# Kernel tuning notes

Hardware: AMD Instinct MI355X
Metric: run time of the kernel (lower is better)

The kernel has to match this reference:

```python
import jax, jax.numpy as jnp
import numpy as np

N_NODES = 100000
N_EDGES = 1600000
D_IN = 128
D_HID = 128
N_GRAPHS = 128


def setup_inputs() -> dict:
    key = jax.random.key(0)
    ks = jax.random.split(key, 6)
    x = jax.random.normal(ks[0], (N_NODES, D_IN), dtype=jnp.float32)
    edge_index = jax.random.randint(ks[1], (2, N_EDGES), 0, N_NODES, dtype=jnp.int32)
    batch = jnp.sort(jax.random.randint(ks[2], (N_NODES,), 0, N_GRAPHS, dtype=jnp.int32))
    # GCNConv params (glorot-ish weight, zero bias), PReLU slope init 0.25 per channel
    W = jax.random.normal(ks[3], (D_IN, D_HID), dtype=jnp.float32) / np.float32(np.sqrt(D_IN))
    b = jnp.zeros((D_HID,), dtype=jnp.float32)
    prelu_a = jnp.full((D_HID,), 0.25, dtype=jnp.float32)
    return {"x": x, "edge_index": edge_index, "batch": batch, "W": W, "b": b, "prelu_a": prelu_a}


def reference(x, edge_index, batch, W, b, prelu_a):
    n_nodes = x.shape[0]
    # ---- GCNConv: add self-loops, symmetric deg^-1/2 normalization ----
    h = x @ W  # [N, H]
    loop = jnp.arange(n_nodes, dtype=edge_index.dtype)
    src = jnp.concatenate([edge_index[0], loop])  # [E+N]
    dst = jnp.concatenate([edge_index[1], loop])
    deg = jax.ops.segment_sum(jnp.ones_like(dst, jnp.float32), dst, num_segments=n_nodes)
    dinv = jnp.where(deg > 0, jax.lax.rsqrt(deg), 0.0)  # deg^-1/2 (inf -> 0, as in PyG)
    norm = dinv[src] * dinv[dst]  # [E+N]
    msg = h[src] * norm[:, None]  # gather + scale
    out = jax.ops.segment_sum(msg, dst, num_segments=n_nodes) + b  # scatter-add
    # ---- PReLU (per-channel slope) ----
    out = jnp.where(out > 0, out, prelu_a * out)
    # ---- F.normalize: L2 over dim=1, eps=1e-12 ----
    nrm = jnp.sqrt(jnp.sum(out * out, axis=1, keepdims=True))
    out = out / jnp.maximum(nrm, 1e-12)
    # ---- global_mean_pool over batch ids ----
    cnt = jax.ops.segment_sum(jnp.ones((n_nodes,), jnp.float32), batch, num_segments=N_GRAPHS)
    pooled = jax.ops.segment_sum(out, batch, num_segments=N_GRAPHS) / jnp.maximum(cnt, 1.0)[:, None]
    return pooled  # [N_GRAPHS, D_HID]
```

## Files before the change

kernel.cpp:

```cpp
#include <hip/hip_runtime.h>

#define D 128
#define NG 128
#define CAP 64
#define BIN 128
#define EPB 8192
#define NBMAX 1024

typedef unsigned short ushort_t;
typedef __bf16 bf16x8 __attribute__((ext_vector_type(8)));
typedef float floatx4 __attribute__((ext_vector_type(4)));

static __device__ __forceinline__ unsigned short f2bf(float f) {
    unsigned u = __float_as_uint(f);
    unsigned r = (u + 0x7fffu + ((u >> 16) & 1u)) >> 16;
    return (unsigned short)r;
}
static __device__ __forceinline__ float bflo(unsigned v) { return __uint_as_float(v << 16); }
static __device__ __forceinline__ float bfhi(unsigned v) { return __uint_as_float(v & 0xffff0000u); }
static __device__ __forceinline__ void acc2(float2& a, unsigned v) {
    a.x += __uint_as_float(v << 16);
    a.y += __uint_as_float(v & 0xffff0000u);
}

__global__ __launch_bounds__(256) void k_init(const float* __restrict__ W, ushort_t* __restrict__ Wp,
                                              const int* __restrict__ batch, int N,
                                              float* __restrict__ cntinv, float* __restrict__ out,
                                              int* __restrict__ cursor, int nb, int cap) {
    int t = blockIdx.x * 256 + threadIdx.x;
    int T = gridDim.x * 256;
    for (int i = t; i < NG * D; i += T) out[i] = 0.f;
    for (int b = t; b < nb; b += T) cursor[b] = b * cap;
    if (blockIdx.x == 0) {
        int tid = threadIdx.x;
        for (int i = tid; i < D * D; i += 256) {
            int c = i >> 7, k = i & 127;
            Wp[i] = f2bf(W[k * D + c]);
        }
        if (tid < NG) {
            int g = tid;
            int lo = 0, hi = N;
            while (lo < hi) { int mid = (lo + hi) >> 1; if (batch[mid] < g) lo = mid + 1; else hi = mid; }
            int a = lo;
            hi = N;
            while (lo < hi) { int mid = (lo + hi) >> 1; if (batch[mid] < g + 1) lo = mid + 1; else hi = mid; }
            int c = lo - a;
            cntinv[g] = 1.0f / (float)(c > 1 ? c : 1);
        }
    }
}

__global__ __launch_bounds__(256) void k_ascatter(const int* __restrict__ src, const int* __restrict__ dst,
                                                  int E, int nb, int* __restrict__ cursor,
                                                  int* __restrict__ ebuf) {
    __shared__ int hist[NBMAX];
    __shared__ int curs[NBMAX];
    int tid = threadIdx.x;
    for (int i = tid; i < nb; i += 256) hist[i] = 0;
    __syncthreads();
    int base = blockIdx.x * EPB;
    int cnt = E - base; if (cnt > EPB) cnt = EPB;
    for (int k = tid; k < cnt; k += 256) {
        atomicAdd(&hist[(unsigned)dst[base + k] >> 7], 1);
    }
    __syncthreads();
    for (int i = tid; i < nb; i += 256) {
        int v = hist[i];
        curs[i] = v ? atomicAdd(&cursor[i], v) : 0;
    }
    __syncthreads();
    for (int k = tid; k < cnt; k += 256) {
        int dv = dst[base + k];
        int sv = src[base + k];
        int pos = atomicAdd(&curs[dv >> 7], 1);
        ebuf[pos] = (sv << 7) | ((dv & 127) << 24);
    }
}

__global__ __launch_bounds__(256) void k_bucket(int* __restrict__ ebuf, const int* __restrict__ cursor,
                                                int cap, int N, int* __restrict__ rs, int* __restrict__ deg) {
    __shared__ int lists[BIN * CAP];
    __shared__ int lcnt[BIN];
    __shared__ int lpos[BIN];
    int tid = threadIdx.x;
    int b = blockIdx.x;
    for (int i = tid; i < BIN; i += 256) lcnt[i] = 0;
    __syncthreads();
    int s = b * cap;
    int e = cursor[b];
    for (int i = s + tid; i < e; i += 256) {
        int pk = ebuf[i];
        int n = (unsigned)pk >> 24;
        int pos = atomicAdd(&lcnt[n], 1);
        if (pos < CAP) lists[n * CAP + pos] = pk & 0xFFFFFF;
    }
    __syncthreads();
    int c0 = (tid < BIN) ? min(lcnt[tid], CAP) : 0;
    if (tid < BIN) lpos[tid] = c0;
    __syncthreads();
    for (int off = 1; off < BIN; off <<= 1) {
        int tv = 0;
        if (tid < BIN && tid >= off) tv = lpos[tid - off];
        __syncthreads();
        if (tid < BIN) lpos[tid] += tv;
        __syncthreads();
    }
    int n0 = b * BIN;
    if (tid < BIN) {
        int node = n0 + tid;
        if (node < N) { rs[node] = s + lpos[tid] - c0; deg[node] = c0; }
    }
    __syncthreads();
    {
        int n = tid >> 1, hf = tid & 1;
        int c = min(lcnt[n], CAP);
        int wbase = s + lpos[n] - c;
        for (int k = hf; k < c; k += 2) ebuf[wbase + k] = lists[n * CAP + k] << 1;
    }
}

__global__ __launch_bounds__(256) void k_gemm(const float* __restrict__ x, const ushort_t* __restrict__ Wp,
                                              const int* __restrict__ deg, ushort_t* __restrict__ h, int N) {
    __shared__ ushort_t smem[64 * 132 + 128 * 128];
    ushort_t* xs = smem;
    ushort_t* ws = smem + 64 * 132;

    const int tid = threadIdx.x;
    const int w = tid >> 6;
    const int lane = tid & 63;
    const int q = lane >> 4;
    const int m = lane & 15;
    const int row0 = blockIdx.x * 64;

#pragma unroll
    for (int it = 0; it < 8; ++it) {
        int i = it * 256 + tid;
        int r = i >> 5, s = i & 31;
        int row = row0 + r;
        uint2 pk;
        if (row < N) {
            float4 v = *(const float4*)&x[(size_t)row * D + s * 4];
            pk.x = (unsigned)f2bf(v.x) | ((unsigned)f2bf(v.y) << 16);
            pk.y = (unsigned)f2bf(v.z) | ((unsigned)f2bf(v.w) << 16);
        } else {
            pk.x = 0; pk.y = 0;
        }
        int off = (s * 8) ^ ((r & 7) << 4);
        *(uint2*)((char*)xs + r * 256 + off) = pk;
    }
#pragma unroll
    for (int it = 0; it < 8; ++it) {
        int i = it * 256 + tid;
        int c = i >> 4, s = i & 15;
        bf16x8 v = *(const bf16x8*)(Wp + (size_t)c * D + s * 8);
        int off = (s * 16) ^ ((c & 7) << 4);
        *(bf16x8*)((char*)ws + c * 256 + off) = v;
    }
    __syncthreads();

    floatx4 acc[8];
#pragma unroll
    for (int nt = 0; nt < 8; ++nt) acc[nt] = (floatx4){0.f, 0.f, 0.f, 0.f};

    const int arow_l = w * 16 + m;
    const int swz = (m & 7) << 4;
#pragma unroll
    for (int kb = 0; kb < 4; ++kb) {
        const int koff = (kb * 64 + q * 16) ^ swz;
        const bf16x8 av = *(const bf16x8*)((const char*)xs + arow_l * 256 + koff);
#pragma unroll
        for (int nt = 0; nt < 8; ++nt) {
            int c = nt * 16 + m;
            const bf16x8 bv = *(const bf16x8*)((const char*)ws + c * 256 + koff);
            acc[nt] = __builtin_amdgcn_mfma_f32_16x16x32_bf16(av, bv, acc[nt], 0, 0, 0);
        }
    }

    float di[4];
#pragma unroll
    for (int r = 0; r < 4; ++r) {
        int row = row0 + w * 16 + q * 4 + r;
        di[r] = (row < N) ? rsqrtf((float)(deg[row] + 1)) : 0.f;
    }
    __syncthreads();

#pragma unroll
    for (int nt = 0; nt < 8; ++nt) {
#pragma unroll
        for (int r = 0; r < 4; ++r) {
            xs[(w * 16 + q * 4 + r) * 132 + nt * 16 + m] = f2bf(acc[nt][r] * di[r]);
        }
    }
    __syncthreads();
#pragma unroll
    for (int it = 0; it < 8; ++it) {
        int i = it * 256 + tid;
        int r = i >> 5, s = i & 31;
        int row = row0 + r;
        if (row < N) {
            *(uint2*)&h[(size_t)row * D + s * 4] = *(const uint2*)&xs[r * 132 + s * 4];
        }
    }
}

__global__ __launch_bounds__(256) void k_gather(const ushort_t* __restrict__ h,
                                                const int* __restrict__ rs, const int* __restrict__ deg,
                                                const int* __restrict__ ebuf,
                                                const int* __restrict__ batch, const float* __restrict__ b,
                                                const float* __restrict__ pa, const float* __restrict__ cntinv,
                                                float* __restrict__ out, int N) {
    __shared__ float rows[4][128];
    __shared__ int gids[4];
    const int wave = threadIdx.x >> 6;
    const int lane = threadIdx.x & 63;
    const int half = lane >> 5;
    const int fl = lane & 31;
    const int node = blockIdx.x * 4 + wave;
    const int nodeC = (node < N) ? node : (N - 1);
    const bool valid = (node < N);
    const char* hb = (const char*)h;
    const unsigned flb = (unsigned)fl * 8;

    float2 a01 = {0.f, 0.f}, a23 = {0.f, 0.f};

    int start = valid ? rs[nodeC] : 0;
    int len = valid ? deg[nodeC] : 0;
    {
        int m = len;
        int idx = (lane < len) ? ebuf[start + lane] : 0;
        int j = 0;
        for (; j + 8 <= m; j += 8) {
            unsigned o0 = (unsigned)__shfl(idx, j + half) + flb;
            unsigned o1 = (unsigned)__shfl(idx, j + 2 + half) + flb;
            unsigned o2 = (unsigned)__shfl(idx, j + 4 + half) + flb;
            unsigned o3 = (unsigned)__shfl(idx, j + 6 + half) + flb;
            uint2 v0 = *(const uint2*)(hb + o0);
            uint2 v1 = *(const uint2*)(hb + o1);
            uint2 v2 = *(const uint2*)(hb + o2);
            uint2 v3 = *(const uint2*)(hb + o3);
            acc2(a01, v0.x); acc2(a23, v0.y);
            acc2(a01, v1.x); acc2(a23, v1.y);
            acc2(a01, v2.x); acc2(a23, v2.y);
            acc2(a01, v3.x); acc2(a23, v3.y);
        }
        for (; j + 2 <= m; j += 2) {
            unsigned o0 = (unsigned)__shfl(idx, j + half) + flb;
            uint2 v0 = *(const uint2*)(hb + o0);
            acc2(a01, v0.x); acc2(a23, v0.y);
        }
        if (j < m) {
            unsigned o0 = (unsigned)__shfl(idx, j) + flb;
            if (half == 0) {
                uint2 v0 = *(const uint2*)(hb + o0);
                acc2(a01, v0.x); acc2(a23, v0.y);
            }
        }
    }

    a01.x += __shfl_xor(a01.x, 32);
    a01.y += __shfl_xor(a01.y, 32);
    a23.x += __shfl_xor(a23.x, 32);
    a23.y += __shfl_xor(a23.y, 32);

    uint2 sv = *(const uint2*)&h[(size_t)nodeC * D + fl * 4];
    acc2(a01, sv.x); acc2(a23, sv.y);

    float dinv = rsqrtf((float)(len + 1));
    float4 bb = *(const float4*)&b[fl * 4];
    float4 aa = *(const float4*)&pa[fl * 4];
    float v0 = a01.x * dinv + bb.x;
    float v1 = a01.y * dinv + bb.y;
    float v2 = a23.x * dinv + bb.z;
    float v3 = a23.y * dinv + bb.w;
    v0 = v0 > 0.f ? v0 : aa.x * v0;
    v1 = v1 > 0.f ? v1 : aa.y * v1;
    v2 = v2 > 0.f ? v2 : aa.z * v2;
    v3 = v3 > 0.f ? v3 : aa.w * v3;
    float ss = v0 * v0 + v1 * v1 + v2 * v2 + v3 * v3;
#pragma unroll
    for (int o = 16; o > 0; o >>= 1) ss += __shfl_xor(ss, o);
    float inv = valid ? (1.0f / fmaxf(sqrtf(ss), 1e-12f)) : 0.f;

    if (half == 0) {
        *(float4*)&rows[wave][fl * 4] = make_float4(v0 * inv, v1 * inv, v2 * inv, v3 * inv);
        if (fl == 0) gids[wave] = batch[nodeC];
    }
    __syncthreads();

    if (threadIdx.x < 128) {
        int f = threadIdx.x;
        float acc = rows[0][f];
        int g = gids[0];
#pragma unroll
        for (int i = 1; i < 4; ++i) {
            int gi = gids[i];
            float vv = rows[i][f];
            if (gi == g) {
                acc += vv;
            } else {
                atomicAdd(&out[(size_t)g * D + f], acc * cntinv[g]);
                g = gi;
                acc = vv;
            }
        }
        atomicAdd(&out[(size_t)g * D + f], acc * cntinv[g]);
    }
}

extern "C" void kernel_launch(void* const* d_in, const int* in_sizes, int n_in,
                              void* d_out, int out_size, void* d_ws, size_t ws_size,
                              hipStream_t stream) {
    const float* x = (const float*)d_in[0];
    const int* ei = (const int*)d_in[1];
    const int* batch = (const int*)d_in[2];
    const float* W = (const float*)d_in[3];
    const float* b = (const float*)d_in[4];
    const float* pa = (const float*)d_in[5];
    float* out = (float*)d_out;

    const int N = in_sizes[0] / D;
    const int E = in_sizes[1] / 2;
    const int* src = ei;
    const int* dst = ei + E;

    const int nb = (N + BIN - 1) / BIN;
    const int nblk = (E + EPB - 1) / EPB;
    const int mean = (E + nb - 1) / nb;
    const int cap = mean + mean / 5 + 512;

    char* w = (char*)d_ws;
    auto carve = [&](size_t bytes) {
        void* p = (void*)w;
        w += (bytes + 255) & ~(size_t)255;
        return p;
    };
    ushort_t* h = (ushort_t*)carve((size_t)N * D * sizeof(ushort_t));
    ushort_t* Wp = (ushort_t*)carve((size_t)D * D * sizeof(ushort_t));
    int* deg = (int*)carve((size_t)N * sizeof(int));
    int* rs = (int*)carve((size_t)N * sizeof(int));
    int* ebuf = (int*)carve((size_t)nb * cap * sizeof(int));
    int* cursor = (int*)carve(NBMAX * sizeof(int));
    float* cntinv = (float*)carve(NG * sizeof(float));

    k_init<<<32, 256, 0, stream>>>(W, Wp, batch, N, cntinv, out, cursor, nb, cap);
    k_ascatter<<<nblk, 256, 0, stream>>>(src, dst, E, nb, cursor, ebuf);
    k_bucket<<<nb, 256, 0, stream>>>(ebuf, cursor, cap, N, rs, deg);
    k_gemm<<<(N + 63) / 64, 256, 0, stream>>>(x, Wp, deg, h, N);
    k_gather<<<(N + 3) / 4, 256, 0, stream>>>(h, rs, deg, ebuf, batch, b, pa, cntinv, out, N);
}
```

Before: 244.4 us.

## Pad edge lists to multiples of eight and map one node per half-wave

The bucket kernel now pads each node's edge list to a multiple of 8 entries. The padding entries point to an extra all-zero row appended to h, which k_init clears. The gather kernel assigns one node to each 32-lane half-wave, so a block handles 8 nodes. Every node then runs fixed 8-wide unrolled load batches with no tail handling and no cross-half reduction. The change also halves edges per scatter block, runs the bucket kernel with 512 threads, and enlarges the per-bin capacity to make room for the padding, at the cost of extra loads of the dummy row.

```diff
diff --git a/kernel.cpp b/kernel.cpp
--- a/kernel.cpp
+++ b/kernel.cpp
@@ -4,7 +4,7 @@
 #define NG 128
 #define CAP 64
 #define BIN 128
-#define EPB 8192
+#define EPB 4096
 #define NBMAX 1024
 
 typedef unsigned short ushort_t;
@@ -16,8 +16,6 @@
     unsigned r = (u + 0x7fffu + ((u >> 16) & 1u)) >> 16;
     return (unsigned short)r;
 }
-static __device__ __forceinline__ float bflo(unsigned v) { return __uint_as_float(v << 16); }
-static __device__ __forceinline__ float bfhi(unsigned v) { return __uint_as_float(v & 0xffff0000u); }
 static __device__ __forceinline__ void acc2(float2& a, unsigned v) {
     a.x += __uint_as_float(v << 16);
     a.y += __uint_as_float(v & 0xffff0000u);
@@ -26,11 +24,13 @@
 __global__ __launch_bounds__(256) void k_init(const float* __restrict__ W, ushort_t* __restrict__ Wp,
                                               const int* __restrict__ batch, int N,
                                               float* __restrict__ cntinv, float* __restrict__ out,
-                                              int* __restrict__ cursor, int nb, int cap) {
+                                              int* __restrict__ cursor, int nb, int cap,
+                                              ushort_t* __restrict__ h) {
     int t = blockIdx.x * 256 + threadIdx.x;
     int T = gridDim.x * 256;
     for (int i = t; i < NG * D; i += T) out[i] = 0.f;
     for (int b = t; b < nb; b += T) cursor[b] = b * cap;
+    for (int i = t; i < D; i += T) h[(size_t)N * D + i] = 0;
     if (blockIdx.x == 0) {
         int tid = threadIdx.x;
         for (int i = tid; i < D * D; i += 256) {
@@ -77,26 +77,30 @@
     }
 }
 
-__global__ __launch_bounds__(256) void k_bucket(int* __restrict__ ebuf, const int* __restrict__ cursor,
+__global__ __launch_bounds__(512) void k_bucket(int* __restrict__ ebuf, const int* __restrict__ cursor,
                                                 int cap, int N, int* __restrict__ rs, int* __restrict__ deg) {
     __shared__ int lists[BIN * CAP];
     __shared__ int lcnt[BIN];
     __shared__ int lpos[BIN];
     int tid = threadIdx.x;
     int b = blockIdx.x;
-    for (int i = tid; i < BIN; i += 256) lcnt[i] = 0;
+    if (tid < BIN) lcnt[tid] = 0;
     __syncthreads();
     int s = b * cap;
     int e = cursor[b];
-    for (int i = s + tid; i < e; i += 256) {
+    for (int i = s + tid; i < e; i += 512) {
         int pk = ebuf[i];
         int n = (unsigned)pk >> 24;
         int pos = atomicAdd(&lcnt[n], 1);
         if (pos < CAP) lists[n * CAP + pos] = pk & 0xFFFFFF;
     }
     __syncthreads();
-    int c0 = (tid < BIN) ? min(lcnt[tid], CAP) : 0;
-    if (tid < BIN) lpos[tid] = c0;
+    int c0 = 0, cp0 = 0;
+    if (tid < BIN) {
+        c0 = min(lcnt[tid], CAP);
+        cp0 = (c0 + 7) & ~7;
+        lpos[tid] = cp0;
+    }
     __syncthreads();
     for (int off = 1; off < BIN; off <<= 1) {
         int tv = 0;
@@ -108,14 +112,17 @@
     int n0 = b * BIN;
     if (tid < BIN) {
         int node = n0 + tid;
-        if (node < N) { rs[node] = s + lpos[tid] - c0; deg[node] = c0; }
+        if (node < N) { rs[node] = s + lpos[tid] - cp0; deg[node] = c0; }
     }
     __syncthreads();
     {
-        int n = tid >> 1, hf = tid & 1;
+        int n = tid >> 2, hf = tid & 3;
         int c = min(lcnt[n], CAP);
-        int wbase = s + lpos[n] - c;
-        for (int k = hf; k < c; k += 2) ebuf[wbase + k] = lists[n * CAP + k] << 1;
+        int cp = (c + 7) & ~7;
+        int wbase = s + lpos[n] - cp;
+        for (int k = hf; k < cp; k += 4) {
+            ebuf[wbase + k] = (k < c) ? (lists[n * CAP + k] << 1) : (N << 8);
+        }
     }
 }
 
@@ -209,60 +216,84 @@
                                                 const int* __restrict__ batch, const float* __restrict__ b,
                                                 const float* __restrict__ pa, const float* __restrict__ cntinv,
                                                 float* __restrict__ out, int N) {
-    __shared__ float rows[4][128];
-    __shared__ int gids[4];
+    __shared__ float rows[8][128];
+    __shared__ int gids[8];
     const int wave = threadIdx.x >> 6;
     const int lane = threadIdx.x & 63;
     const int half = lane >> 5;
     const int fl = lane & 31;
-    const int node = blockIdx.x * 4 + wave;
-    const int nodeC = (node < N) ? node : (N - 1);
+    const int hb = half << 5;
+    const int node = blockIdx.x * 8 + wave * 2 + half;
     const bool valid = (node < N);
-    const char* hb = (const char*)h;
+    const int nodeC = valid ? node : (N - 1);
+    const char* hp = (const char*)h;
     const unsigned flb = (unsigned)fl * 8;
 
     float2 a01 = {0.f, 0.f}, a23 = {0.f, 0.f};
 
-    int start = valid ? rs[nodeC] : 0;
+    int start = rs[nodeC];
     int len = valid ? deg[nodeC] : 0;
-    {
-        int m = len;
-        int idx = (lane < len) ? ebuf[start + lane] : 0;
-        int j = 0;
-        for (; j + 8 <= m; j += 8) {
-            unsigned o0 = (unsigned)__shfl(idx, j + half) + flb;
-            unsigned o1 = (unsigned)__shfl(idx, j + 2 + half) + flb;
-            unsigned o2 = (unsigned)__shfl(idx, j + 4 + half) + flb;
-            unsigned o3 = (unsigned)__shfl(idx, j + 6 + half) + flb;
-            uint2 v0 = *(const uint2*)(hb + o0);
-            uint2 v1 = *(const uint2*)(hb + o1);
-            uint2 v2 = *(const uint2*)(hb + o2);
-            uint2 v3 = *(const uint2*)(hb + o3);
+    int lenp = (len + 7) & ~7;
+
+    unsigned idxA = (fl < lenp) ? (unsigned)ebuf[start + fl] : 0;
+    int j1 = lenp < 32 ? lenp : 32;
+    for (int j = 0; j < j1; j += 8) {
+        unsigned o0 = __shfl(idxA, hb + j + 0) + flb;
+        unsigned o1 = __shfl(idxA, hb + j + 1) + flb;
+        unsigned o2 = __shfl(idxA, hb + j + 2) + flb;
+        unsigned o3 = __shfl(idxA, hb + j + 3) + flb;
+        unsigned o4 = __shfl(idxA, hb + j + 4) + flb;
+        unsigned o5 = __shfl(idxA, hb + j + 5) + flb;
+        unsigned o6 = __shfl(idxA, hb + j + 6) + flb;
+        unsigned o7 = __shfl(idxA, hb + j + 7) + flb;
+        uint2 v0 = *(const uint2*)(hp + o0);
+        uint2 v1 = *(const uint2*)(hp + o1);
+        uint2 v2 = *(const uint2*)(hp + o2);
+        uint2 v3 = *(const uint2*)(hp + o3);
+        uint2 v4 = *(const uint2*)(hp + o4);
+        uint2 v5 = *(const uint2*)(hp + o5);
+        uint2 v6 = *(const uint2*)(hp + o6);
+        uint2 v7 = *(const uint2*)(hp + o7);
+        acc2(a01, v0.x); acc2(a23, v0.y);
+        acc2(a01, v1.x); acc2(a23, v1.y);
+        acc2(a01, v2.x); acc2(a23, v2.y);
+        acc2(a01, v3.x); acc2(a23, v3.y);
+        acc2(a01, v4.x); acc2(a23, v4.y);
+        acc2(a01, v5.x); acc2(a23, v5.y);
+        acc2(a01, v6.x); acc2(a23, v6.y);
+        acc2(a01, v7.x); acc2(a23, v7.y);
+    }
+    if (lenp > 32) {
+        unsigned idxB = (32 + fl < lenp) ? (unsigned)ebuf[start + 32 + fl] : 0;
+        for (int j = 32; j < lenp; j += 8) {
+            unsigned o0 = __shfl(idxB, hb + j - 32 + 0) + flb;
+            unsigned o1 = __shfl(idxB, hb + j - 32 + 1) + flb;
+            unsigned o2 = __shfl(idxB, hb + j - 32 + 2) + flb;
+            unsigned o3 = __shfl(idxB, hb + j - 32 + 3) + flb;
+            unsigned o4 = __shfl(idxB, hb + j - 32 + 4) + flb;
+            unsigned o5 = __shfl(idxB, hb + j - 32 + 5) + flb;
+            unsigned o6 = __shfl(idxB, hb + j - 32 + 6) + flb;
+            unsigned o7 = __shfl(idxB, hb + j - 32 + 7) + flb;
+            uint2 v0 = *(const uint2*)(hp + o0);
+            uint2 v1 = *(const uint2*)(hp + o1);
+            uint2 v2 = *(const uint2*)(hp + o2);
+            uint2 v3 = *(const uint2*)(hp + o3);
+            uint2 v4 = *(const uint2*)(hp + o4);
+            uint2 v5 = *(const uint2*)(hp + o5);
+            uint2 v6 = *(const uint2*)(hp + o6);
+            uint2 v7 = *(const uint2*)(hp + o7);
             acc2(a01, v0.x); acc2(a23, v0.y);
             acc2(a01, v1.x); acc2(a23, v1.y);
             acc2(a01, v2.x); acc2(a23, v2.y);
             acc2(a01, v3.x); acc2(a23, v3.y);
-        }
-        for (; j + 2 <= m; j += 2) {
-            unsigned o0 = (unsigned)__shfl(idx, j + half) + flb;
-            uint2 v0 = *(const uint2*)(hb + o0);
-            acc2(a01, v0.x); acc2(a23, v0.y);
-        }
-        if (j < m) {
-            unsigned o0 = (unsigned)__shfl(idx, j) + flb;
-            if (half == 0) {
-                uint2 v0 = *(const uint2*)(hb + o0);
-                acc2(a01, v0.x); acc2(a23, v0.y);
-            }
-        }
-    }
-
-    a01.x += __shfl_xor(a01.x, 32);
-    a01.y += __shfl_xor(a01.y, 32);
-    a23.x += __shfl_xor(a23.x, 32);
-    a23.y += __shfl_xor(a23.y, 32);
-
-    uint2 sv = *(const uint2*)&h[(size_t)nodeC * D + fl * 4];
+            acc2(a01, v4.x); acc2(a23, v4.y);
+            acc2(a01, v5.x); acc2(a23, v5.y);
+            acc2(a01, v6.x); acc2(a23, v6.y);
+            acc2(a01, v7.x); acc2(a23, v7.y);
+        }
+    }
+
+    uint2 sv = *(const uint2*)(hp + (unsigned)nodeC * 256 + flb);
     acc2(a01, sv.x); acc2(a23, sv.y);
 
     float dinv = rsqrtf((float)(len + 1));
@@ -281,10 +312,8 @@
     for (int o = 16; o > 0; o >>= 1) ss += __shfl_xor(ss, o);
     float inv = valid ? (1.0f / fmaxf(sqrtf(ss), 1e-12f)) : 0.f;
 
-    if (half == 0) {
-        *(float4*)&rows[wave][fl * 4] = make_float4(v0 * inv, v1 * inv, v2 * inv, v3 * inv);
-        if (fl == 0) gids[wave] = batch[nodeC];
-    }
+    *(float4*)&rows[wave * 2 + half][fl * 4] = make_float4(v0 * inv, v1 * inv, v2 * inv, v3 * inv);
+    if (fl == 0) gids[wave * 2 + half] = valid ? batch[node] : -1;
     __syncthreads();
 
     if (threadIdx.x < 128) {
@@ -292,18 +321,18 @@
         float acc = rows[0][f];
         int g = gids[0];
 #pragma unroll
-        for (int i = 1; i < 4; ++i) {
+        for (int i = 1; i < 8; ++i) {
             int gi = gids[i];
             float vv = rows[i][f];
             if (gi == g) {
                 acc += vv;
             } else {
-                atomicAdd(&out[(size_t)g * D + f], acc * cntinv[g]);
+                if (g >= 0) atomicAdd(&out[(size_t)g * D + f], acc * cntinv[g]);
                 g = gi;
                 acc = vv;
             }
         }
-        atomicAdd(&out[(size_t)g * D + f], acc * cntinv[g]);
+        if (g >= 0) atomicAdd(&out[(size_t)g * D + f], acc * cntinv[g]);
     }
 }
 
@@ -326,7 +355,7 @@
     const int nb = (N + BIN - 1) / BIN;
     const int nblk = (E + EPB - 1) / EPB;
     const int mean = (E + nb - 1) / nb;
-    const int cap = mean + mean / 5 + 512;
+    const int cap = mean + mean / 2 + 640;
 
     char* w = (char*)d_ws;
     auto carve = [&](size_t bytes) {
@@ -334,7 +363,7 @@
         w += (bytes + 255) & ~(size_t)255;
         return p;
     };
-    ushort_t* h = (ushort_t*)carve((size_t)N * D * sizeof(ushort_t));
+    ushort_t* h = (ushort_t*)carve((size_t)(N + 1) * D * sizeof(ushort_t));
     ushort_t* Wp = (ushort_t*)carve((size_t)D * D * sizeof(ushort_t));
     int* deg = (int*)carve((size_t)N * sizeof(int));
     int* rs = (int*)carve((size_t)N * sizeof(int));
@@ -342,9 +371,9 @@
     int* cursor = (int*)carve(NBMAX * sizeof(int));
     float* cntinv = (float*)carve(NG * sizeof(float));
 
-    k_init<<<32, 256, 0, stream>>>(W, Wp, batch, N, cntinv, out, cursor, nb, cap);
+    k_init<<<32, 256, 0, stream>>>(W, Wp, batch, N, cntinv, out, cursor, nb, cap, h);
     k_ascatter<<<nblk, 256, 0, stream>>>(src, dst, E, nb, cursor, ebuf);
-    k_bucket<<<nb, 256, 0, stream>>>(ebuf, cursor, cap, N, rs, deg);
+    k_bucket<<<nb, 512, 0, stream>>>(ebuf, cursor, cap, N, rs, deg);
     k_gemm<<<(N + 63) / 64, 256, 0, stream>>>(x, Wp, deg, h, N);
-    k_gather<<<(N + 3) / 4, 256, 0, stream>>>(h, rs, deg, ebuf, batch, b, pa, cntinv, out, N);
-}
+    k_gather<<<(N + 7) / 8, 256, 0, stream>>>(h, rs, deg, ebuf, batch, b, pa, cntinv, out, N);
+}
```

Measured after the change: 223.2 us. 1.09x faster.
